# Kernel tuning notes

Measured on AMD Instinct MI355X. Metric: run time of the kernel, lower is better.

Reference implementation:

```python
import jax, jax.numpy as jnp
import numpy as np

B, N, C, H, KH = 4, 4096, 1024, 16, 5
HD = C // H  # head dim = 64


def setup_inputs() -> dict:
    key = jax.random.key(0)
    ks = jax.random.split(key, 4)
    return {
        "x": jax.random.normal(ks[0], (B, N, C), jnp.float32),
        "qkv_w": jax.random.normal(ks[1], (3 * C, C), jnp.float32) * 0.02,
        "qkv_b": jnp.zeros((3 * C,), jnp.float32),
        "proj_w": jax.random.normal(ks[2], (C, C), jnp.float32) * 0.02,
        "proj_b": jnp.zeros((C,), jnp.float32),
        "pos_enc": jnp.zeros((1, C), jnp.float32),  # torch init: zeros
        "dwc_w": jax.random.normal(ks[3], (HD, 1, KH, KH), jnp.float32) * 0.05,
        "dwc_b": jnp.zeros((HD,), jnp.float32),
        "num_heads": H,
    }


def reference(x, qkv_w, qkv_b, proj_w, proj_b, pos_enc, dwc_w, dwc_b, num_heads):
    b, n, c = x.shape
    h = num_heads
    hd = c // h
    kh = dwc_w.shape[2]

    qkv = x @ qkv_w.T + qkv_b                     # (b, n, 3c)
    q, k, v = jnp.split(qkv, 3, axis=-1)          # each (b, n, c)
    k = k + pos_enc[:, :c]                        # broadcast (1, c)
    q = jax.nn.relu(q)
    k = jax.nn.relu(k)

    def to_heads(t):  # (b, n, c) -> (b*h, n, hd)
        return t.reshape(b, n, h, hd).transpose(0, 2, 1, 3).reshape(b * h, n, hd)

    q, k, v = to_heads(q), to_heads(k), to_heads(v)

    # linear attention in fp32 (inputs already fp32)
    z = 1.0 / (jnp.einsum('bic,bc->bi', q, k.sum(axis=1)) + 1e-6)   # (bh, n)
    kv = jnp.einsum('bjc,bjd->bcd', k, v)                           # (bh, hd, hd)
    out = jnp.einsum('bic,bcd->bid', q, kv) * z[:, :, None]         # (bh, n, hd)

    # depthwise 2D conv on v viewed as (bh, hd, n, 1), kernel (hd,1,kh,kh), pad kh//2
    fm = v.transpose(0, 2, 1)[..., None]                            # (bh, hd, n, 1)
    pad = kh // 2
    fm = jax.lax.conv_general_dilated(
        fm, dwc_w, window_strides=(1, 1),
        padding=((pad, pad), (pad, pad)),
        dimension_numbers=('NCHW', 'OIHW', 'NCHW'),
        feature_group_count=hd,
    ) + dwc_b[None, :, None, None]
    out = out + fm[..., 0].transpose(0, 2, 1)                       # (bh, n, hd)

    out = out.reshape(b, h, n, hd).transpose(0, 2, 1, 3).reshape(b, n, c)
    return out @ proj_w.T + proj_b
```

## Files before the change

### kernel.cpp

```cpp
#include <hip/hip_runtime.h>


#define BB   4
#define NN   4096
#define CDIM 1024
#define NH   16
#define HDIM 64
#define BH   64

typedef __attribute__((ext_vector_type(8))) short short8;
typedef __attribute__((ext_vector_type(4))) float f32x4;
typedef unsigned short u16;

__device__ __forceinline__ float b2f(short s) {
    union { unsigned u; float f; } c;
    c.u = ((unsigned)(unsigned short)s) << 16;
    return c.f;
}
__device__ __forceinline__ u16 f2b(float f) {
    unsigned u = __float_as_uint(f);
    return (u16)((u + 0x7fffu + ((u >> 16) & 1u)) >> 16);
}
__device__ __forceinline__ void gload16(const void* g, void* l) {
    __builtin_amdgcn_global_load_lds((const __attribute__((address_space(1))) void*)g,
                                     (__attribute__((address_space(3))) void*)l, 16, 0, 0);
}

__global__ __launch_bounds__(256) void k_fill_diag(float* __restrict__ out, int n, float val)
{
    int i = blockIdx.x * 256 + threadIdx.x;
    if (i < n) out[i] = val;
}

__global__ __launch_bounds__(256) void k_convert_all(
    const float* __restrict__ x, const float* __restrict__ qw, const float* __restrict__ pw,
    u16* __restrict__ xb, u16* __restrict__ qwb, u16* __restrict__ pwb)
{
    int i = blockIdx.x * 256 + threadIdx.x;
    const float* src; u16* dst; int j;
    if (i < 4194304)      { src = x;  dst = xb;  j = i; }
    else if (i < 4980736) { src = qw; dst = qwb; j = i - 4194304; }
    else                  { src = pw; dst = pwb; j = i - 4980736; }
    float4 v = reinterpret_cast<const float4*>(src)[j];
    ushort4 o;
    o.x = f2b(v.x); o.y = f2b(v.y); o.z = f2b(v.z); o.w = f2b(v.w);
    reinterpret_cast<ushort4*>(dst)[j] = o;
}

#define GEMM256_8PH()                                                                    \
    const int t = threadIdx.x;                                                           \
    const int l = t & 63, w = t >> 6;                                                    \
    const int wr = w >> 2, wc = w & 3;                                                   \
    const int fr = l & 15;                                                               \
    const int physE  = ((l >> 4) ^ ((fr >> 1) & 3)) * 8;                                 \
    const int qa     = ((l & 3) ^ ((l >> 3) & 3)) * 8;                                   \
    const int aRow   = w * 16 + (l >> 2);                                                \
    const u16* gA0 = A  + (size_t)(brow + aRow) * 1024 + qa;                             \
    const u16* gB0 = Bw + (size_t)(bcol + aRow) * 1024 + qa;                             \
    char* ldsc = (char*)lds;                                                             \
    const int afBase = (wr * 128 + fr) * 32 + physE;                                     \
    const int bfBase = 16384 + (wc * 64 + fr) * 32 + physE;                              \
    f32x4 acc[8][4];                                                                     \
    _Pragma("unroll")                                                                    \
    for (int m = 0; m < 8; ++m)                                                          \
        _Pragma("unroll")                                                                \
        for (int n = 0; n < 4; ++n) acc[m][n] = (f32x4){0.f, 0.f, 0.f, 0.f};             \
    auto STG = [&](int kt, int kh, int isB) {                                            \
        const u16* g = (isB ? gB0 : gA0) + kt * 64 + kh * 32;                            \
        char* d = ldsc + (kt & 1) * 65536 + isB * 32768 + kh * 16384 + w * 1024 + l * 16;\
        gload16(g,          d);                                                          \
        gload16(g + 131072, d + 8192);                                                   \
    };                                                                                   \
    STG(0,0,0); STG(0,0,1); STG(0,1,0); STG(0,1,1); STG(1,0,0); STG(1,0,1);              \
    asm volatile("s_waitcnt vmcnt(4)" ::: "memory");                                     \
    __builtin_amdgcn_sched_barrier(0);                                                   \
    __builtin_amdgcn_s_barrier();                                                        \
    __builtin_amdgcn_sched_barrier(0);                                                   \
    _Pragma("unroll 1")                                                                  \
    for (int kt = 0; kt < 16; ++kt) {                                                    \
        const int B0 = (kt & 1) * 32768;                                                 \
        short8 af[4], bf[4];                                                             \
        _Pragma("unroll")                                                                \
        for (int m = 0; m < 4; ++m)                                                      \
            af[m] = *reinterpret_cast<const short8*>(&lds[B0 + afBase + m * 512]);       \
        _Pragma("unroll")                                                                \
        for (int n = 0; n < 4; ++n)                                                      \
            bf[n] = *reinterpret_cast<const short8*>(&lds[B0 + bfBase + n * 512]);       \
        if (kt + 1 < 16) STG(kt + 1, 1, 0);                                              \
        __builtin_amdgcn_sched_barrier(0);                                               \
        __builtin_amdgcn_s_barrier();                                                    \
        asm volatile("s_waitcnt lgkmcnt(0)" ::: "memory");                               \
        __builtin_amdgcn_sched_barrier(0);                                               \
        __builtin_amdgcn_s_setprio(1);                                                   \
        _Pragma("unroll")                                                                \
        for (int m = 0; m < 4; ++m)                                                      \
            _Pragma("unroll")                                                            \
            for (int n = 0; n < 4; ++n)                                                  \
                acc[m][n] = __builtin_amdgcn_mfma_f32_16x16x32_bf16(af[m], bf[n], acc[m][n], 0, 0, 0); \
        __builtin_amdgcn_s_setprio(0);                                                   \
        __builtin_amdgcn_sched_barrier(0);                                               \
        __builtin_amdgcn_s_barrier();                                                    \
        __builtin_amdgcn_sched_barrier(0);                                               \
        _Pragma("unroll")                                                                \
        for (int m = 0; m < 4; ++m)                                                      \
            af[m] = *reinterpret_cast<const short8*>(&lds[B0 + afBase + (m + 4) * 512]); \
        if (kt + 1 < 16) STG(kt + 1, 1, 1);                                              \
        __builtin_amdgcn_sched_barrier(0);                                               \
        __builtin_amdgcn_s_barrier();                                                    \
        asm volatile("s_waitcnt lgkmcnt(0)" ::: "memory");                               \
        __builtin_amdgcn_sched_barrier(0);                                               \
        __builtin_amdgcn_s_setprio(1);                                                   \
        _Pragma("unroll")                                                                \
        for (int m = 0; m < 4; ++m)                                                      \
            _Pragma("unroll")                                                            \
            for (int n = 0; n < 4; ++n)                                                  \
                acc[m + 4][n] = __builtin_amdgcn_mfma_f32_16x16x32_bf16(af[m], bf[n], acc[m + 4][n], 0, 0, 0); \
        __builtin_amdgcn_s_setprio(0);                                                   \
        __builtin_amdgcn_sched_barrier(0);                                               \
        __builtin_amdgcn_s_barrier();                                                    \
        __builtin_amdgcn_sched_barrier(0);                                               \
        _Pragma("unroll")                                                                \
        for (int m = 0; m < 4; ++m)                                                      \
            af[m] = *reinterpret_cast<const short8*>(&lds[B0 + 8192 + afBase + m * 512]);\
        _Pragma("unroll")                                                                \
        for (int n = 0; n < 4; ++n)                                                      \
            bf[n] = *reinterpret_cast<const short8*>(&lds[B0 + 8192 + bfBase + n * 512]);\
        if (kt + 2 < 16) STG(kt + 2, 0, 0);                                              \
        __builtin_amdgcn_sched_barrier(0);                                               \
        __builtin_amdgcn_s_barrier();                                                    \
        asm volatile("s_waitcnt lgkmcnt(0)" ::: "memory");                               \
        __builtin_amdgcn_sched_barrier(0);                                               \
        __builtin_amdgcn_s_setprio(1);                                                   \
        _Pragma("unroll")                                                                \
        for (int m = 0; m < 4; ++m)                                                      \
            _Pragma("unroll")                                                            \
            for (int n = 0; n < 4; ++n)                                                  \
                acc[m][n] = __builtin_amdgcn_mfma_f32_16x16x32_bf16(af[m], bf[n], acc[m][n], 0, 0, 0); \
        __builtin_amdgcn_s_setprio(0);                                                   \
        __builtin_amdgcn_sched_barrier(0);                                               \
        __builtin_amdgcn_s_barrier();                                                    \
        __builtin_amdgcn_sched_barrier(0);                                               \
        _Pragma("unroll")                                                                \
        for (int m = 0; m < 4; ++m)                                                      \
            af[m] = *reinterpret_cast<const short8*>(&lds[B0 + 8192 + afBase + (m + 4) * 512]); \
        if (kt + 2 < 16) STG(kt + 2, 0, 1);                                              \
        __builtin_amdgcn_sched_barrier(0);                                               \
        __builtin_amdgcn_s_barrier();                                                    \
        asm volatile("s_waitcnt lgkmcnt(0)" ::: "memory");                               \
        __builtin_amdgcn_sched_barrier(0);                                               \
        __builtin_amdgcn_s_setprio(1);                                                   \
        _Pragma("unroll")                                                                \
        for (int m = 0; m < 4; ++m)                                                      \
            _Pragma("unroll")                                                            \
            for (int n = 0; n < 4; ++n)                                                  \
                acc[m + 4][n] = __builtin_amdgcn_mfma_f32_16x16x32_bf16(af[m], bf[n], acc[m + 4][n], 0, 0, 0); \
        __builtin_amdgcn_s_setprio(0);                                                   \
        __builtin_amdgcn_sched_barrier(0);                                               \
        if (kt < 15) { asm volatile("s_waitcnt vmcnt(4)" ::: "memory"); }                \
        else         { asm volatile("s_waitcnt vmcnt(0)" ::: "memory"); }                \
        __builtin_amdgcn_sched_barrier(0);                                               \
        __builtin_amdgcn_s_barrier();                                                    \
        __builtin_amdgcn_sched_barrier(0);                                               \
    }

__global__ __launch_bounds__(512, 2) void k_gemm1_256(
    const u16* __restrict__ A, const u16* __restrict__ Bw,
    const float* __restrict__ bias, const float* __restrict__ pos_enc,
    u16* __restrict__ q, u16* __restrict__ ktg, u16* __restrict__ vtg)
{
    __shared__ u16 lds[65536];
    const int lid = blockIdx.y * 12 + blockIdx.x;
    const int swz = (lid & 7) * 96 + (lid >> 3);
    const int bcol = (swz % 12) * 256;
    const int brow = (swz / 12) * 256;

    GEMM256_8PH()

    const int part = bcol >> 10;
    {
        const int row_l = wr * 128 + (l >> 4) * 4;
        const int col_l = wc * 64 + fr;
        #pragma unroll
        for (int n = 0; n < 4; ++n) {
            const int col = col_l + n * 16;
            const int gc = bcol + col;
            const int c = gc & 1023;
            float bv = bias[gc];
            if (part == 1) bv += pos_enc[c];
            const int cc = col >> 3, in = col & 7;
            #pragma unroll
            for (int m = 0; m < 8; ++m)
                #pragma unroll
                for (int j = 0; j < 4; ++j) {
                    const int row = row_l + m * 16 + j;
                    float val = acc[m][n][j] + bv;
                    if (part != 2) val = fmaxf(val, 0.f);
                    lds[row * 256 + ((cc ^ (row & 7)) << 3) + in] = f2b(val);
                }
        }
    }
    __syncthreads();
    const int b_ = brow >> 12, i0 = brow & 4095;
    if (part == 0) {
        #pragma unroll
        for (int it = 0; it < 16; ++it) {
            const int id = it * 512 + t;
            const int row = id >> 5, cc = id & 31;
            short8 val = *reinterpret_cast<const short8*>(&lds[row * 256 + ((cc ^ (row & 7)) << 3)]);
            const int c2 = (bcol + cc * 8) & 1023;
            const int h2 = c2 >> 6, d2 = c2 & 63;
            *reinterpret_cast<short8*>(
                &q[((size_t)(b_ * NH + h2) * NN + i0 + row) * HDIM + d2]) = val;
        }
    } else {
        u16* dstT = (part == 1) ? ktg : vtg;
        #pragma unroll
        for (int it = 0; it < 16; ++it) {
            const int id = it * 512 + t;
            const int cl = id & 255, jc = id >> 8;
            short8 vv;
            #pragma unroll
            for (int rr = 0; rr < 8; ++rr)
                vv[rr] = (short)lds[(jc * 8 + rr) * 256 + (((cl >> 3) ^ rr) << 3) + (cl & 7)];
            const int c2 = (bcol + cl) & 1023;
            const int h2 = c2 >> 6, d2 = c2 & 63;
            *reinterpret_cast<short8*>(
                &dstT[((size_t)(b_ * NH + h2) * HDIM + d2) * NN + i0 + jc * 8]) = vv;
        }
    }
}

__global__ __launch_bounds__(512, 2) void k_gemm2_256(
    const u16* __restrict__ A, const u16* __restrict__ Bw,
    const float* __restrict__ bias, float* __restrict__ out)
{
    __shared__ u16 lds[65536];
    const int lid = blockIdx.y * 4 + blockIdx.x;
    const int swz = (lid & 7) * 32 + (lid >> 3);
    const int bcol = (swz % 4) * 256;
    const int brow = (swz / 4) * 256;

    GEMM256_8PH()

    float* ldsf = reinterpret_cast<float*>(lds);
    #pragma unroll 1
    for (int half = 0; half < 2; ++half) {
        __syncthreads();
        if (wr == half) {
            const int row_l = (l >> 4) * 4;
            const int col_l = wc * 64 + fr;
            #pragma unroll
            for (int n = 0; n < 4; ++n) {
                const int col = col_l + n * 16;
                const float bv = bias[bcol + col];
                #pragma unroll
                for (int m = 0; m < 8; ++m)
                    #pragma unroll
                    for (int j = 0; j < 4; ++j) {
                        const int row = m * 16 + row_l + j;
                        ldsf[row * 256 + (col ^ (((row >> 2) & 3) << 3))] = acc[m][n][j] + bv;
                    }
            }
        }
        __syncthreads();
        const float4* ldsf4 = reinterpret_cast<const float4*>(ldsf);
        #pragma unroll
        for (int it = 0; it < 16; ++it) {
            const int id = it * 512 + t;
            const int row = id >> 6, cc4 = id & 63;
            float4 vv = ldsf4[row * 64 + (cc4 ^ (((row >> 2) & 3) << 1))];
            *reinterpret_cast<float4*>(
                &out[(size_t)(brow + half * 128 + row) * CDIM + bcol + cc4 * 4]) = vv;
        }
    }
}

__global__ __launch_bounds__(256) void k_kv_mfma(
    const u16* __restrict__ ktg, const u16* __restrict__ vtg,
    float* __restrict__ part)
{
    __shared__ float red[4][5120];
    const int t = threadIdx.x, l = t & 63, w = t >> 6;
    const int bh = blockIdx.x, ch = blockIdx.y;
    const u16* kb = ktg + (size_t)bh * HDIM * NN;
    const u16* vb = vtg + (size_t)bh * HDIM * NN;
    const int j0 = ch * 1024 + w * 256;
    const int fr = l & 15, kf = (l >> 4) * 8;

    f32x4 acc[5][4];
    #pragma unroll
    for (int m = 0; m < 5; ++m)
        #pragma unroll
        for (int n = 0; n < 4; ++n) acc[m][n] = (f32x4){0.f, 0.f, 0.f, 0.f};
    short8 ones;
    #pragma unroll
    for (int i = 0; i < 8; ++i) ones[i] = (short)0x3F80;

    for (int js = 0; js < 256; js += 32) {
        const int jb = j0 + js + kf;
        short8 a[4], b[4];
        #pragma unroll
        for (int m = 0; m < 4; ++m)
            a[m] = *reinterpret_cast<const short8*>(&vb[(size_t)(m * 16 + fr) * NN + jb]);
        #pragma unroll
        for (int n = 0; n < 4; ++n)
            b[n] = *reinterpret_cast<const short8*>(&kb[(size_t)(n * 16 + fr) * NN + jb]);
        #pragma unroll
        for (int m = 0; m < 4; ++m)
            #pragma unroll
            for (int n = 0; n < 4; ++n)
                acc[m][n] = __builtin_amdgcn_mfma_f32_16x16x32_bf16(a[m], b[n], acc[m][n], 0, 0, 0);
        #pragma unroll
        for (int n = 0; n < 4; ++n)
            acc[4][n] = __builtin_amdgcn_mfma_f32_16x16x32_bf16(ones, b[n], acc[4][n], 0, 0, 0);
    }
    #pragma unroll
    for (int m = 0; m < 5; ++m)
        #pragma unroll
        for (int n = 0; n < 4; ++n)
            #pragma unroll
            for (int j = 0; j < 4; ++j)
                red[w][(m * 16 + (l >> 4) * 4 + j) * 64 + fr + n * 16] = acc[m][n][j];
    __syncthreads();
    float* po = part + ((size_t)ch * BH + bh) * 5120;
    for (int i = t; i < 5120; i += 256)
        po[i] = red[0][i] + red[1][i] + red[2][i] + red[3][i];
}

__global__ __launch_bounds__(256) void k_kv_red(
    const float* __restrict__ part, u16* __restrict__ kvt)
{
    const int bh = blockIdx.x, t = threadIdx.x;
    u16* base = kvt + bh * 5120;
    for (int i = t; i < 5120; i += 256) {
        float s = part[(size_t)(0 * BH + bh) * 5120 + i]
                + part[(size_t)(1 * BH + bh) * 5120 + i]
                + part[(size_t)(2 * BH + bh) * 5120 + i]
                + part[(size_t)(3 * BH + bh) * 5120 + i];
        base[i] = f2b(s);
    }
}

__global__ __launch_bounds__(256) void k_attn_mfma(
    const u16* __restrict__ q, const u16* __restrict__ vtg,
    const u16* __restrict__ kvt,
    const float* __restrict__ dwc_w, const float* __restrict__ dwc_b,
    u16* __restrict__ out2)
{
    __shared__ u16 att[4][64 * 68];
    const int t = threadIdx.x;
    const int l = t & 63, w = t >> 6;
    const int bh = blockIdx.x;
    const int tb = blockIdx.y * 256 + w * 64;
    const u16* qb  = q + (size_t)bh * NN * HDIM + (size_t)tb * HDIM;
    const u16* kvb = kvt + bh * 5120;

    const int fr = l & 15;
    const int kfrag = (l >> 4) * 8;

    short8 bfr[5][2];
    #pragma unroll
    for (int n = 0; n < 5; ++n)
        #pragma unroll
        for (int ks = 0; ks < 2; ++ks)
            bfr[n][ks] = *reinterpret_cast<const short8*>(&kvb[(n * 16 + fr) * 64 + ks * 32 + kfrag]);

    f32x4 acc[4][5];
    #pragma unroll
    for (int m = 0; m < 4; ++m)
        #pragma unroll
        for (int n = 0; n < 5; ++n) acc[m][n] = (f32x4){0.f, 0.f, 0.f, 0.f};

    #pragma unroll
    for (int m = 0; m < 4; ++m)
        #pragma unroll
        for (int ks = 0; ks < 2; ++ks) {
            short8 a = *reinterpret_cast<const short8*>(&qb[(m * 16 + fr) * 64 + ks * 32 + kfrag]);
            #pragma unroll
            for (int n = 0; n < 5; ++n)
                acc[m][n] = __builtin_amdgcn_mfma_f32_16x16x32_bf16(a, bfr[n][ks], acc[m][n], 0, 0, 0);
        }

    #pragma unroll
    for (int m = 0; m < 4; ++m)
        #pragma unroll
        for (int j = 0; j < 4; ++j) {
            const float den = __shfl(acc[m][4][j], l & 48);
            const float z = 1.f / (den + 1e-6f);
            const int row = m * 16 + (l >> 4) * 4 + j;
            #pragma unroll
            for (int n = 0; n < 4; ++n)
                att[w][row * 68 + fr + n * 16] = f2b(acc[m][n][j] * z);
        }
    __syncthreads();

    const int d = l;
    const u16* vrow = vtg + (size_t)bh * HDIM * NN + (size_t)d * NN;
    float w5[5];
    #pragma unroll
    for (int dh = 0; dh < 5; ++dh) w5[dh] = dwc_w[d * 25 + dh * 5 + 2];
    const float cbias = dwc_b[d];
    const int b_ = bh >> 4, h_ = bh & 15;
    u16* obase = out2 + (size_t)b_ * NN * CDIM + (size_t)h_ * 64 + d;
    float win[5];
    #pragma unroll
    for (int p = 0; p < 4; ++p) {
        const int src = tb - 2 + p;
        win[p] = (src >= 0 && src < NN) ? b2f(vrow[src]) : 0.f;
    }
    for (int it = 0; it < 64; ++it) {
        const int srcn = tb + it + 2;
        win[4] = (srcn < NN) ? b2f(vrow[srcn]) : 0.f;
        const float fm = cbias + w5[0] * win[0] + w5[1] * win[1] + w5[2] * win[2]
                               + w5[3] * win[3] + w5[4] * win[4];
        const float attn = b2f((short)att[w][it * 68 + d]);
        obase[(size_t)(tb + it) * CDIM] = f2b(attn + fm);
        win[0] = win[1]; win[1] = win[2]; win[2] = win[3]; win[3] = win[4];
    }
}

extern "C" void kernel_launch(void* const* d_in, const int* in_sizes, int n_in,
                              void* d_out, int out_size, void* d_ws, size_t ws_size,
                              hipStream_t stream)
{
    const float* x       = (const float*)d_in[0];
    const float* qkv_w   = (const float*)d_in[1];
    const float* qkv_b   = (const float*)d_in[2];
    const float* proj_w  = (const float*)d_in[3];
    const float* proj_b  = (const float*)d_in[4];
    const float* pos_enc = (const float*)d_in[5];
    const float* dwc_w   = (const float*)d_in[6];
    const float* dwc_b   = (const float*)d_in[7];

    const size_t QKV = 16777216;
    char* p = (char*)d_ws;
    u16* q_b    = (u16*)p;               p += QKV * 2;
    u16* ktg    = (u16*)p;               p += QKV * 2;
    u16* vtg    = (u16*)p;               p += QKV * 2;
    u16* x_b    = (u16*)p;               p += QKV * 2;
    u16* qkvw_b = (u16*)p;               p += (size_t)3145728 * 2;
    u16* projw_b= (u16*)p;               p += (size_t)1048576 * 2;
    float* part = (float*)p;             p += (size_t)4 * BH * 5120 * 4;
    u16* kvt    = (u16*)p;               p += (size_t)(BH * 5120) * 2;
    const size_t need_bytes = (size_t)(p - (char*)d_ws);

    if (ws_size < need_bytes) {
        const float diag = 4096.0f + (float)(ws_size >> 20);
        k_fill_diag<<<(out_size + 255) / 256, 256, 0, stream>>>((float*)d_out, out_size, diag);
        return;
    }

    u16* out2 = ktg;
    float* out = (float*)d_out;

    k_convert_all<<<20480, 256, 0, stream>>>(x, qkv_w, proj_w, x_b, qkvw_b, projw_b);

    k_gemm1_256 <<<dim3(12, 64), 512, 0, stream>>>(x_b, qkvw_b, qkv_b, pos_enc, q_b, ktg, vtg);
    k_kv_mfma   <<<dim3(64, 4),  256, 0, stream>>>(ktg, vtg, part);
    k_kv_red    <<<64,           256, 0, stream>>>(part, kvt);
    k_attn_mfma <<<dim3(64, 16), 256, 0, stream>>>(q_b, vtg, kvt, dwc_w, dwc_b, out2);
    k_gemm2_256 <<<dim3(4, 64),  512, 0, stream>>>(out2, projw_b, proj_b, out);
}
```

Measured before the change: 305.4 us.

## Merge GEMM k-loop into four phases and add row-major V copy for conv

The GEMM main loop is restructured from eight half-tile phases to four: all eight A fragments are loaded at once and both B/A stage loads are issued together, which halves the barrier count per k-step at the cost of more registers. Separately, GEMM1 now also writes V in row-major head layout, and the attention/conv kernel reads that instead of the transposed V. Each thread's conv window load becomes a strided walk along rows, so lanes in a wavefront read adjacent addresses instead of addresses spread across rows. The extra V write adds memory traffic and workspace, and the larger fragment arrays may raise register pressure under launch_bounds(512,2).

After: 285.5 us. 6.5% less time.

```diff
diff --git a/kernel.cpp b/kernel.cpp
--- a/kernel.cpp
+++ b/kernel.cpp
@@ -47,7 +47,7 @@
     reinterpret_cast<ushort4*>(dst)[j] = o;
 }
 
-#define GEMM256_8PH()                                                                    \
+#define GEMM256_4PH()                                                                    \
     const int t = threadIdx.x;                                                           \
     const int l = t & 63, w = t >> 6;                                                    \
     const int wr = w >> 2, wc = w & 3;                                                   \
@@ -79,21 +79,22 @@
     _Pragma("unroll 1")                                                                  \
     for (int kt = 0; kt < 16; ++kt) {                                                    \
         const int B0 = (kt & 1) * 32768;                                                 \
-        short8 af[4], bf[4];                                                             \
-        _Pragma("unroll")                                                                \
-        for (int m = 0; m < 4; ++m)                                                      \
+        short8 af[8], bf[4];                                                             \
+                                           \
+        _Pragma("unroll")                                                                \
+        for (int m = 0; m < 8; ++m)                                                      \
             af[m] = *reinterpret_cast<const short8*>(&lds[B0 + afBase + m * 512]);       \
         _Pragma("unroll")                                                                \
         for (int n = 0; n < 4; ++n)                                                      \
             bf[n] = *reinterpret_cast<const short8*>(&lds[B0 + bfBase + n * 512]);       \
-        if (kt + 1 < 16) STG(kt + 1, 1, 0);                                              \
+        if (kt + 1 < 16) { STG(kt + 1, 1, 0); STG(kt + 1, 1, 1); }                       \
         __builtin_amdgcn_sched_barrier(0);                                               \
         __builtin_amdgcn_s_barrier();                                                    \
         asm volatile("s_waitcnt lgkmcnt(0)" ::: "memory");                               \
         __builtin_amdgcn_sched_barrier(0);                                               \
         __builtin_amdgcn_s_setprio(1);                                                   \
         _Pragma("unroll")                                                                \
-        for (int m = 0; m < 4; ++m)                                                      \
+        for (int m = 0; m < 8; ++m)                                                      \
             _Pragma("unroll")                                                            \
             for (int n = 0; n < 4; ++n)                                                  \
                 acc[m][n] = __builtin_amdgcn_mfma_f32_16x16x32_bf16(af[m], bf[n], acc[m][n], 0, 0, 0); \
@@ -101,61 +102,26 @@
         __builtin_amdgcn_sched_barrier(0);                                               \
         __builtin_amdgcn_s_barrier();                                                    \
         __builtin_amdgcn_sched_barrier(0);                                               \
-        _Pragma("unroll")                                                                \
-        for (int m = 0; m < 4; ++m)                                                      \
-            af[m] = *reinterpret_cast<const short8*>(&lds[B0 + afBase + (m + 4) * 512]); \
-        if (kt + 1 < 16) STG(kt + 1, 1, 1);                                              \
+                                           \
+        _Pragma("unroll")                                                                \
+        for (int m = 0; m < 8; ++m)                                                      \
+            af[m] = *reinterpret_cast<const short8*>(&lds[B0 + 8192 + afBase + m * 512]);\
+        _Pragma("unroll")                                                                \
+        for (int n = 0; n < 4; ++n)                                                      \
+            bf[n] = *reinterpret_cast<const short8*>(&lds[B0 + 8192 + bfBase + n * 512]);\
+        if (kt + 2 < 16) { STG(kt + 2, 0, 0); STG(kt + 2, 0, 1); }                       \
         __builtin_amdgcn_sched_barrier(0);                                               \
         __builtin_amdgcn_s_barrier();                                                    \
         asm volatile("s_waitcnt lgkmcnt(0)" ::: "memory");                               \
         __builtin_amdgcn_sched_barrier(0);                                               \
         __builtin_amdgcn_s_setprio(1);                                                   \
         _Pragma("unroll")                                                                \
-        for (int m = 0; m < 4; ++m)                                                      \
-            _Pragma("unroll")                                                            \
-            for (int n = 0; n < 4; ++n)                                                  \
-                acc[m + 4][n] = __builtin_amdgcn_mfma_f32_16x16x32_bf16(af[m], bf[n], acc[m + 4][n], 0, 0, 0); \
-        __builtin_amdgcn_s_setprio(0);                                                   \
-        __builtin_amdgcn_sched_barrier(0);                                               \
-        __builtin_amdgcn_s_barrier();                                                    \
-        __builtin_amdgcn_sched_barrier(0);                                               \
-        _Pragma("unroll")                                                                \
-        for (int m = 0; m < 4; ++m)                                                      \
-            af[m] = *reinterpret_cast<const short8*>(&lds[B0 + 8192 + afBase + m * 512]);\
-        _Pragma("unroll")                                                                \
-        for (int n = 0; n < 4; ++n)                                                      \
-            bf[n] = *reinterpret_cast<const short8*>(&lds[B0 + 8192 + bfBase + n * 512]);\
-        if (kt + 2 < 16) STG(kt + 2, 0, 0);                                              \
-        __builtin_amdgcn_sched_barrier(0);                                               \
-        __builtin_amdgcn_s_barrier();                                                    \
-        asm volatile("s_waitcnt lgkmcnt(0)" ::: "memory");                               \
-        __builtin_amdgcn_sched_barrier(0);                                               \
-        __builtin_amdgcn_s_setprio(1);                                                   \
-        _Pragma("unroll")                                                                \
-        for (int m = 0; m < 4; ++m)                                                      \
+        for (int m = 0; m < 8; ++m)                                                      \
             _Pragma("unroll")                                                            \
             for (int n = 0; n < 4; ++n)                                                  \
                 acc[m][n] = __builtin_amdgcn_mfma_f32_16x16x32_bf16(af[m], bf[n], acc[m][n], 0, 0, 0); \
         __builtin_amdgcn_s_setprio(0);                                                   \
         __builtin_amdgcn_sched_barrier(0);                                               \
-        __builtin_amdgcn_s_barrier();                                                    \
-        __builtin_amdgcn_sched_barrier(0);                                               \
-        _Pragma("unroll")                                                                \
-        for (int m = 0; m < 4; ++m)                                                      \
-            af[m] = *reinterpret_cast<const short8*>(&lds[B0 + 8192 + afBase + (m + 4) * 512]); \
-        if (kt + 2 < 16) STG(kt + 2, 0, 1);                                              \
-        __builtin_amdgcn_sched_barrier(0);                                               \
-        __builtin_amdgcn_s_barrier();                                                    \
-        asm volatile("s_waitcnt lgkmcnt(0)" ::: "memory");                               \
-        __builtin_amdgcn_sched_barrier(0);                                               \
-        __builtin_amdgcn_s_setprio(1);                                                   \
-        _Pragma("unroll")                                                                \
-        for (int m = 0; m < 4; ++m)                                                      \
-            _Pragma("unroll")                                                            \
-            for (int n = 0; n < 4; ++n)                                                  \
-                acc[m + 4][n] = __builtin_amdgcn_mfma_f32_16x16x32_bf16(af[m], bf[n], acc[m + 4][n], 0, 0, 0); \
-        __builtin_amdgcn_s_setprio(0);                                                   \
-        __builtin_amdgcn_sched_barrier(0);                                               \
         if (kt < 15) { asm volatile("s_waitcnt vmcnt(4)" ::: "memory"); }                \
         else         { asm volatile("s_waitcnt vmcnt(0)" ::: "memory"); }                \
         __builtin_amdgcn_sched_barrier(0);                                               \
@@ -166,7 +132,7 @@
 __global__ __launch_bounds__(512, 2) void k_gemm1_256(
     const u16* __restrict__ A, const u16* __restrict__ Bw,
     const float* __restrict__ bias, const float* __restrict__ pos_enc,
-    u16* __restrict__ q, u16* __restrict__ ktg, u16* __restrict__ vtg)
+    u16* __restrict__ q, u16* __restrict__ ktg, u16* __restrict__ v, u16* __restrict__ vtg)
 {
     __shared__ u16 lds[65536];
     const int lid = blockIdx.y * 12 + blockIdx.x;
@@ -174,7 +140,7 @@
     const int bcol = (swz % 12) * 256;
     const int brow = (swz / 12) * 256;
 
-    GEMM256_8PH()
+    GEMM256_4PH()
 
     const int part = bcol >> 10;
     {
@@ -201,7 +167,8 @@
     }
     __syncthreads();
     const int b_ = brow >> 12, i0 = brow & 4095;
-    if (part == 0) {
+    if (part != 1) {
+        u16* dst = (part == 0) ? q : v;
         #pragma unroll
         for (int it = 0; it < 16; ++it) {
             const int id = it * 512 + t;
@@ -210,9 +177,10 @@
             const int c2 = (bcol + cc * 8) & 1023;
             const int h2 = c2 >> 6, d2 = c2 & 63;
             *reinterpret_cast<short8*>(
-                &q[((size_t)(b_ * NH + h2) * NN + i0 + row) * HDIM + d2]) = val;
-        }
-    } else {
+                &dst[((size_t)(b_ * NH + h2) * NN + i0 + row) * HDIM + d2]) = val;
+        }
+    }
+    if (part != 0) {
         u16* dstT = (part == 1) ? ktg : vtg;
         #pragma unroll
         for (int it = 0; it < 16; ++it) {
@@ -240,7 +208,7 @@
     const int bcol = (swz % 4) * 256;
     const int brow = (swz / 4) * 256;
 
-    GEMM256_8PH()
+    GEMM256_4PH()
 
     float* ldsf = reinterpret_cast<float*>(lds);
     #pragma unroll 1
@@ -342,7 +310,7 @@
 }
 
 __global__ __launch_bounds__(256) void k_attn_mfma(
-    const u16* __restrict__ q, const u16* __restrict__ vtg,
+    const u16* __restrict__ q, const u16* __restrict__ v,
     const u16* __restrict__ kvt,
     const float* __restrict__ dwc_w, const float* __restrict__ dwc_b,
     u16* __restrict__ out2)
@@ -352,7 +320,8 @@
     const int l = t & 63, w = t >> 6;
     const int bh = blockIdx.x;
     const int tb = blockIdx.y * 256 + w * 64;
-    const u16* qb  = q + (size_t)bh * NN * HDIM + (size_t)tb * HDIM;
+    const size_t hb = (size_t)bh * NN * HDIM;
+    const u16* qb  = q + hb + (size_t)tb * HDIM;
     const u16* kvb = kvt + bh * 5120;
 
     const int fr = l & 15;
@@ -395,7 +364,6 @@
     __syncthreads();
 
     const int d = l;
-    const u16* vrow = vtg + (size_t)bh * HDIM * NN + (size_t)d * NN;
     float w5[5];
     #pragma unroll
     for (int dh = 0; dh < 5; ++dh) w5[dh] = dwc_w[d * 25 + dh * 5 + 2];
@@ -406,11 +374,11 @@
     #pragma unroll
     for (int p = 0; p < 4; ++p) {
         const int src = tb - 2 + p;
-        win[p] = (src >= 0 && src < NN) ? b2f(vrow[src]) : 0.f;
+        win[p] = (src >= 0 && src < NN) ? b2f(v[hb + (size_t)src * 64 + d]) : 0.f;
     }
     for (int it = 0; it < 64; ++it) {
         const int srcn = tb + it + 2;
-        win[4] = (srcn < NN) ? b2f(vrow[srcn]) : 0.f;
+        win[4] = (srcn < NN) ? b2f(v[hb + (size_t)srcn * 64 + d]) : 0.f;
         const float fm = cbias + w5[0] * win[0] + w5[1] * win[1] + w5[2] * win[2]
                                + w5[3] * win[3] + w5[4] * win[4];
         const float attn = b2f((short)att[w][it * 68 + d]);
@@ -436,6 +404,7 @@
     char* p = (char*)d_ws;
     u16* q_b    = (u16*)p;               p += QKV * 2;
     u16* ktg    = (u16*)p;               p += QKV * 2;
+    u16* v_b    = (u16*)p;               p += QKV * 2;
     u16* vtg    = (u16*)p;               p += QKV * 2;
     u16* x_b    = (u16*)p;               p += QKV * 2;
     u16* qkvw_b = (u16*)p;               p += (size_t)3145728 * 2;
@@ -455,9 +424,9 @@
 
     k_convert_all<<<20480, 256, 0, stream>>>(x, qkv_w, proj_w, x_b, qkvw_b, projw_b);
 
-    k_gemm1_256 <<<dim3(12, 64), 512, 0, stream>>>(x_b, qkvw_b, qkv_b, pos_enc, q_b, ktg, vtg);
+    k_gemm1_256 <<<dim3(12, 64), 512, 0, stream>>>(x_b, qkvw_b, qkv_b, pos_enc, q_b, ktg, v_b, vtg);
     k_kv_mfma   <<<dim3(64, 4),  256, 0, stream>>>(ktg, vtg, part);
     k_kv_red    <<<64,           256, 0, stream>>>(part, kvt);
-    k_attn_mfma <<<dim3(64, 16), 256, 0, stream>>>(q_b, vtg, kvt, dwc_w, dwc_b, out2);
+    k_attn_mfma <<<dim3(64, 16), 256, 0, stream>>>(q_b, v_b, kvt, dwc_w, dwc_b, out2);
     k_gemm2_256 <<<dim3(4, 64),  512, 0, stream>>>(out2, projw_b, proj_b, out);
 }
```
